# Kernel optimization log

Measured on AMD Instinct MI355X. Metric: run time of the kernel, lower is better.

Reference implementation:

```python
import jax, jax.numpy as jnp
import numpy as np

S = 7
NUM_CLASSES = 20
BATCH = 16384


def _iou(a, b):
    # a, b: [..., 4] boxes in (cx, cy, w, h) format
    ax1, ay1 = a[..., 0] - a[..., 2] / 2, a[..., 1] - a[..., 3] / 2
    ax2, ay2 = a[..., 0] + a[..., 2] / 2, a[..., 1] + a[..., 3] / 2
    bx1, by1 = b[..., 0] - b[..., 2] / 2, b[..., 1] - b[..., 3] / 2
    bx2, by2 = b[..., 0] + b[..., 2] / 2, b[..., 1] + b[..., 3] / 2
    iw = jnp.clip(jnp.minimum(ax2, bx2) - jnp.maximum(ax1, bx1), 0.0)
    ih = jnp.clip(jnp.minimum(ay2, by2) - jnp.maximum(ay1, by1), 0.0)
    inter = iw * ih
    union = a[..., 2] * a[..., 3] + b[..., 2] * b[..., 3] - inter
    return inter / (union + 1e-10)


def setup_inputs() -> dict:
    key = jax.random.key(0)
    k1, k2, k3, k4 = jax.random.split(key, 4)
    preds = jax.random.uniform(k1, (BATCH, S, S, 30), jnp.float32, 0.05, 0.95)
    box = jax.random.uniform(k2, (BATCH, S, S, 4), jnp.float32, 0.05, 0.95)
    conf = jax.random.bernoulli(k3, 0.3, (BATCH, S, S, 1)).astype(jnp.float32)
    cls = jax.random.uniform(k4, (BATCH, S, S, NUM_CLASSES), jnp.float32)
    labels = jnp.concatenate([box, conf, box, conf, cls], axis=-1)
    return {"preds": preds, "labels": labels}


def reference(preds, labels):
    obj = labels[..., 4] == 1.0          # [N, S, S] responsible-cell mask
    obj_f = obj.astype(preds.dtype)
    noobj_f = 1.0 - obj_f

    iou1 = _iou(preds[..., 0:4], labels[..., 0:4])
    iou2 = _iou(preds[..., 5:9], labels[..., 0:4])
    b1 = iou1 > iou2                      # box 1 is responsible
    b1f = b1.astype(preds.dtype)[..., None]

    # responsible / other box slices selected per cell
    p_xy = b1f * preds[..., 0:2] + (1 - b1f) * preds[..., 5:7]
    l_xy = b1f * labels[..., 0:2] + (1 - b1f) * labels[..., 5:7]
    p_wh = b1f * preds[..., 2:4] + (1 - b1f) * preds[..., 7:9]
    l_wh = b1f * labels[..., 2:4] + (1 - b1f) * labels[..., 7:9]
    conf_resp = jnp.where(b1, preds[..., 4], preds[..., 9])
    conf_other = jnp.where(b1, preds[..., 9], preds[..., 4])
    iou_resp = jnp.where(b1, iou1, iou2)
    iou_other = jnp.where(b1, iou2, iou1)

    loss_xy = 5.0 * jnp.sum(obj_f * jnp.sum((p_xy - l_xy) ** 2, axis=-1))
    loss_wh = jnp.sum(obj_f * jnp.sum((jnp.sqrt(p_wh) - jnp.sqrt(l_wh)) ** 2, axis=-1))
    loss_obj = jnp.sum(obj_f * (conf_resp - iou_resp) ** 2)
    loss_noobj_in = 0.5 * jnp.sum(obj_f * (conf_other - iou_other) ** 2)
    loss_noobj_out = 0.5 * jnp.sum(noobj_f * (preds[..., 4] ** 2 + preds[..., 9] ** 2))
    loss_cls = jnp.sum(obj_f * jnp.sum((preds[..., 10:] - labels[..., 10:]) ** 2, axis=-1))

    total = loss_xy + loss_wh + loss_obj + loss_noobj_in + loss_noobj_out + loss_cls
    return total / preds.shape[0]
```

## Files before the change

kernel.cpp:

```cpp
#include <hip/hip_runtime.h>

#define S 7
#define NUM_CLASSES 20
#define BATCH 16384
#define NCELLS (BATCH * S * S)
#define BLOCK 256

__device__ __forceinline__ float iou_f(float acx, float acy, float aw, float ah,
                                       float bcx, float bcy, float bw, float bh) {
    float ax1 = acx - aw * 0.5f, ay1 = acy - ah * 0.5f;
    float ax2 = acx + aw * 0.5f, ay2 = acy + ah * 0.5f;
    float bx1 = bcx - bw * 0.5f, by1 = bcy - bh * 0.5f;
    float bx2 = bcx + bw * 0.5f, by2 = bcy + bh * 0.5f;
    float iw = fminf(ax2, bx2) - fmaxf(ax1, bx1);
    iw = fmaxf(iw, 0.0f);
    float ih = fminf(ay2, by2) - fmaxf(ay1, by1);
    ih = fmaxf(ih, 0.0f);
    float inter = iw * ih;
    float uni = aw * ah + bw * bh - inter;
    return inter / (uni + 1e-10f);
}

__global__ void zero_out_kernel(float* out) {
    out[0] = 0.0f;
}

__global__ __launch_bounds__(BLOCK) void yolo_loss_kernel(
        const float* __restrict__ preds,
        const float* __restrict__ labels,
        float* __restrict__ out) {
    int cell = blockIdx.x * BLOCK + threadIdx.x;

    float p[30], l[30];
    const float2* pp = (const float2*)(preds + (size_t)cell * 30);
    const float2* ll = (const float2*)(labels + (size_t)cell * 30);
#pragma unroll
    for (int j = 0; j < 15; ++j) {
        float2 v = pp[j];
        p[2 * j] = v.x; p[2 * j + 1] = v.y;
        float2 w = ll[j];
        l[2 * j] = w.x; l[2 * j + 1] = w.y;
    }

    float obj = (l[4] == 1.0f) ? 1.0f : 0.0f;

    float iou1 = iou_f(p[0], p[1], p[2], p[3], l[0], l[1], l[2], l[3]);
    float iou2 = iou_f(p[5], p[6], p[7], p[8], l[0], l[1], l[2], l[3]);
    bool b1 = iou1 > iou2;

    float pxy0 = b1 ? p[0] : p[5];
    float pxy1 = b1 ? p[1] : p[6];
    float pwh0 = b1 ? p[2] : p[7];
    float pwh1 = b1 ? p[3] : p[8];
    float conf_resp  = b1 ? p[4] : p[9];
    float conf_other = b1 ? p[9] : p[4];
    float iou_resp   = b1 ? iou1 : iou2;
    float iou_other  = b1 ? iou2 : iou1;

    float dx = pxy0 - l[0];
    float dy = pxy1 - l[1];
    float loss_xy = dx * dx + dy * dy;

    float sw0 = sqrtf(pwh0) - sqrtf(l[2]);
    float sw1 = sqrtf(pwh1) - sqrtf(l[3]);
    float loss_wh = sw0 * sw0 + sw1 * sw1;

    float d_obj = conf_resp - iou_resp;
    float loss_obj = d_obj * d_obj;

    float d_no = conf_other - iou_other;
    float loss_noobj_in = 0.5f * d_no * d_no;

    float loss_noobj_out = 0.5f * (1.0f - obj) * (p[4] * p[4] + p[9] * p[9]);

    float loss_cls = 0.0f;
#pragma unroll
    for (int c = 10; c < 30; ++c) {
        float d = p[c] - l[c];
        loss_cls += d * d;
    }

    float loss = obj * (5.0f * loss_xy + loss_wh + loss_obj + loss_noobj_in + loss_cls)
               + loss_noobj_out;

#pragma unroll
    for (int off = 32; off > 0; off >>= 1)
        loss += __shfl_down(loss, off, 64);

    __shared__ float wsum[BLOCK / 64];
    int lane = threadIdx.x & 63;
    int wid  = threadIdx.x >> 6;
    if (lane == 0) wsum[wid] = loss;
    __syncthreads();
    if (threadIdx.x == 0) {
        float s = wsum[0] + wsum[1] + wsum[2] + wsum[3];
        atomicAdd(out, s * (1.0f / (float)BATCH));
    }
}

extern "C" void kernel_launch(void* const* d_in, const int* in_sizes, int n_in,
                              void* d_out, int out_size, void* d_ws, size_t ws_size,
                              hipStream_t stream) {
    const float* preds  = (const float*)d_in[0];
    const float* labels = (const float*)d_in[1];
    float* out = (float*)d_out;

    zero_out_kernel<<<1, 1, 0, stream>>>(out);

    int nblocks = NCELLS / BLOCK;
    yolo_loss_kernel<<<nblocks, BLOCK, 0, stream>>>(preds, labels, out);
}
```

Baseline: 212.9 us.

## Process two cells per thread with float4 loads and two-stage reduction

Each thread now handles two adjacent cells, loading 60 floats from each input with 16-byte vector loads instead of 8-byte loads. It skips the one label float4 group that holds only unused fields of the second cell. Per-block atomics and the zeroing kernel are replaced by per-block partials in workspace plus a single-block reduce kernel. The aim is wider, more efficient memory transactions and no atomic contention, at the cost of more registers per thread, fewer threads, and an extra kernel launch.

```diff
diff --git a/kernel.cpp b/kernel.cpp
--- a/kernel.cpp
+++ b/kernel.cpp
@@ -5,6 +5,9 @@
 #define BATCH 16384
 #define NCELLS (BATCH * S * S)
 #define BLOCK 256
+#define CELLS_PER_THREAD 2
+#define NTHREADS (NCELLS / CELLS_PER_THREAD)
+#define NBLOCKS (NTHREADS / BLOCK)
 
 __device__ __forceinline__ float iou_f(float acx, float acy, float aw, float ah,
                                        float bcx, float bcy, float bw, float bh) {
@@ -21,27 +24,7 @@
     return inter / (uni + 1e-10f);
 }
 
-__global__ void zero_out_kernel(float* out) {
-    out[0] = 0.0f;
-}
-
-__global__ __launch_bounds__(BLOCK) void yolo_loss_kernel(
-        const float* __restrict__ preds,
-        const float* __restrict__ labels,
-        float* __restrict__ out) {
-    int cell = blockIdx.x * BLOCK + threadIdx.x;
-
-    float p[30], l[30];
-    const float2* pp = (const float2*)(preds + (size_t)cell * 30);
-    const float2* ll = (const float2*)(labels + (size_t)cell * 30);
-#pragma unroll
-    for (int j = 0; j < 15; ++j) {
-        float2 v = pp[j];
-        p[2 * j] = v.x; p[2 * j + 1] = v.y;
-        float2 w = ll[j];
-        l[2 * j] = w.x; l[2 * j + 1] = w.y;
-    }
-
+__device__ __forceinline__ float cell_loss(const float* p, const float* l) {
     float obj = (l[4] == 1.0f) ? 1.0f : 0.0f;
 
     float iou1 = iou_f(p[0], p[1], p[2], p[3], l[0], l[1], l[2], l[3]);
@@ -80,8 +63,30 @@
         loss_cls += d * d;
     }
 
-    float loss = obj * (5.0f * loss_xy + loss_wh + loss_obj + loss_noobj_in + loss_cls)
-               + loss_noobj_out;
+    return obj * (5.0f * loss_xy + loss_wh + loss_obj + loss_noobj_in + loss_cls)
+         + loss_noobj_out;
+}
+
+__global__ __launch_bounds__(BLOCK) void yolo_loss_kernel(
+        const float* __restrict__ preds,
+        const float* __restrict__ labels,
+        float* __restrict__ partials) {
+    int t = blockIdx.x * BLOCK + threadIdx.x;
+
+    const float4* P = (const float4*)(preds  + (size_t)t * 60);
+    const float4* L = (const float4*)(labels + (size_t)t * 60);
+
+    float pr[60], lb[60];
+    float4* pr4 = (float4*)pr;
+    float4* lb4 = (float4*)lb;
+
+#pragma unroll
+    for (int g = 0; g < 15; ++g) pr4[g] = P[g];
+#pragma unroll
+    for (int g = 0; g < 15; ++g)
+        if (g != 9) lb4[g] = L[g];
+
+    float loss = cell_loss(pr, lb) + cell_loss(pr + 30, lb + 30);
 
 #pragma unroll
     for (int off = 32; off > 0; off >>= 1)
@@ -92,9 +97,30 @@
     int wid  = threadIdx.x >> 6;
     if (lane == 0) wsum[wid] = loss;
     __syncthreads();
+    if (threadIdx.x == 0)
+        partials[blockIdx.x] = wsum[0] + wsum[1] + wsum[2] + wsum[3];
+}
+
+__global__ __launch_bounds__(1024) void reduce_kernel(
+        const float* __restrict__ partials,
+        float* __restrict__ out) {
+    float s = 0.0f;
+    for (int i = threadIdx.x; i < NBLOCKS; i += 1024)
+        s += partials[i];
+#pragma unroll
+    for (int off = 32; off > 0; off >>= 1)
+        s += __shfl_down(s, off, 64);
+
+    __shared__ float wsum[16];
+    int lane = threadIdx.x & 63;
+    int wid  = threadIdx.x >> 6;
+    if (lane == 0) wsum[wid] = s;
+    __syncthreads();
     if (threadIdx.x == 0) {
-        float s = wsum[0] + wsum[1] + wsum[2] + wsum[3];
-        atomicAdd(out, s * (1.0f / (float)BATCH));
+        float t = 0.0f;
+#pragma unroll
+        for (int w = 0; w < 16; ++w) t += wsum[w];
+        out[0] = t * (1.0f / (float)BATCH);
     }
 }
 
@@ -104,9 +130,8 @@
     const float* preds  = (const float*)d_in[0];
     const float* labels = (const float*)d_in[1];
     float* out = (float*)d_out;
+    float* partials = (float*)d_ws;
 
-    zero_out_kernel<<<1, 1, 0, stream>>>(out);
-
-    int nblocks = NCELLS / BLOCK;
-    yolo_loss_kernel<<<nblocks, BLOCK, 0, stream>>>(preds, labels, out);
+    yolo_loss_kernel<<<NBLOCKS, BLOCK, 0, stream>>>(preds, labels, partials);
+    reduce_kernel<<<1, 1024, 0, stream>>>(partials, out);
 }
```

New measurement: 230.9 us. 1.08x slower.
